# Kernel optimization log

Measured on AMD Instinct MI355X. Metric: run time of the kernel, lower is better.

The kernel has to match this reference:

```python
import jax, jax.numpy as jnp
import numpy as np

B = 4            # number of scenes (equal-size segments; offset = [M,2M,3M,4M])
K_NEAR = 16
K_FAR = 32
K_SMOOTH = 8
T_LOC = 0.1
T_CON = 0.5
BN_EPS = 1e-5


def setup_inputs() -> dict:
    key = jax.random.key(0)
    ks = jax.random.split(key, 8)
    N, C, H, O = 32768, 6, 64, 1
    coords = jax.random.uniform(ks[0], (N, 3), jnp.float32) * 2.0 - 1.0
    feat = jax.random.normal(ks[1], (N, C), jnp.float32)
    return {
        'feat': feat,
        'coords': coords,
        'W1': jax.random.normal(ks[2], (C, H), jnp.float32) * 0.1,
        'b1': jnp.zeros((H,), jnp.float32),
        'g1': jnp.ones((H,), jnp.float32),
        'be1': jnp.zeros((H,), jnp.float32),
        'W2': jax.random.normal(ks[3], (H, H), jnp.float32) * 0.1,
        'b2': jnp.zeros((H,), jnp.float32),
        'g2': jnp.ones((H,), jnp.float32),
        'be2': jnp.zeros((H,), jnp.float32),
        'W3': jax.random.normal(ks[4], (H, O), jnp.float32) * 0.1,
        'b3': jnp.zeros((O,), jnp.float32),
    }


def _bn_train(x, g, b):
    # BatchNorm1d in train mode: biased batch statistics
    mu = x.mean(axis=0)
    var = x.var(axis=0)
    return g * (x - mu) * jax.lax.rsqrt(var + BN_EPS) + b


def _knn_per_scene(c):
    # c: [M,3] -> [M,K_FAR] sorted nearest-neighbor indices (self first)
    sq = jnp.sum(c * c, axis=-1)                       # [M]
    d2 = sq[:, None] + sq[None, :] - 2.0 * (c @ c.T)   # [M,M] GEMM-based
    return jax.lax.top_k(-d2, K_FAR)[1]                # [M,K_FAR]


def _forward(feat, coords, W1, b1, g1, be1, W2, b2, g2, be2, W3, b3):
    N = feat.shape[0]
    M = N // B
    # ---- PointSorter MLP -> ordering scores in (0,1) ----
    h = jax.nn.gelu(_bn_train(feat @ W1 + b1, g1, be1), approximate=False)
    h = jax.nn.gelu(_bn_train(h @ W2 + b2, g2, be2), approximate=False)
    scores = jax.nn.sigmoid(h @ W3 + b3)               # [N, num_orders]
    s = scores.mean(axis=1, keepdims=True)             # [N,1] (scores_mean)
    # ---- single fused KNN (k=32); slice for k=16 (near) and k=8 (smooth) ----
    cb = coords.reshape(B, M, 3)
    idx = jax.vmap(_knn_per_scene)(cb)                 # [B,M,K_FAR] local
    idx = (idx + (jnp.arange(B) * M)[:, None, None]).reshape(N, K_FAR)
    idx_near = idx[:, :K_NEAR]
    idx_far = idx[:, K_NEAR:]
    idx_sm = idx[:, :K_SMOOTH]
    # ---- locality: neighbors should have similar scores ----
    sd = jnp.abs(s[:, None, :] - s[idx_near])[..., 0]          # [N,16]
    diff = coords[:, None, :] - coords[idx_near]               # [N,16,3]
    d = jnp.sqrt(jnp.maximum(jnp.sum(diff * diff, axis=2), 1e-24))
    w = jnp.exp(-d / T_LOC)
    loss_loc = jnp.sum(w * sd * sd) / jnp.maximum(jnp.sum(w), 1e-8)
    # ---- contrastive: far points should have different scores ----
    sim_pos = 1.0 - jnp.abs(s[:, None, :] - s[idx_near])       # [N,16,1]
    sim_neg = 1.0 - jnp.abs(s[:, None, :] - s[idx_far])        # [N,16,1]
    loss_pos = -jnp.mean(jnp.log(jax.nn.sigmoid(sim_pos / T_CON) + 1e-8))
    loss_neg = -jnp.mean(jnp.log(1.0 - jax.nn.sigmoid(sim_neg / T_CON) + 1e-8))
    loss_con = loss_pos + loss_neg
    # ---- smoothness: score close to mean of 8-NN scores ----
    nmean = s[idx_sm].mean(axis=1)                             # [N,1]
    loss_sm = jnp.mean((s - nmean) ** 2)
    return 1.0 * loss_loc + 0.5 * loss_con + 0.2 * loss_sm


def reference(feat, coords, W1, b1, g1, be1, W2, b2, g2, be2, W3, b3):
    return _forward(feat, coords, W1, b1, g1, be1, W2, b2, g2, be2, W3, b3)
```

## Files before the change

### kernel.cpp

```cpp
#include <hip/hip_runtime.h>

typedef unsigned long long u64;
typedef unsigned int u32;
typedef unsigned short u16;

#define N_PTS 32768
#define M_PTS 8192
#define C_IN 6
#define H_DIM 64

#define G 6
#define NCELL 216
#define NCELL_T 864
#define CW (1.0f/3.0f)

#define NBLK 256
#define NBLKD 1024
#define QG 4
#define NTASK (NCELL_T*2)
#define KTGT 48.0f

#define TL0 0.0494f
#define TL1 0.0740f
#define TL2 0.1110f
#define TL3 0.1736f
#define TL4 0.2600f
#define TL5 0.4000f

#define KEYMASK 0xFFFFE000u
#define IDXMASK 0x1FFFu


__device__ __forceinline__ float gelu_exact(float x) {
    return 0.5f * x * (1.0f + erff(x * 0.70710678118654752f));
}
__device__ __forceinline__ float sigmoidf_(float x) {
    return 1.0f / (1.0f + expf(-x));
}

__device__ __forceinline__ u32 bitonic_sort64_u32(u32 key, int lane) {
    #pragma unroll
    for (int k = 2; k <= 64; k <<= 1) {
        #pragma unroll
        for (int j = k >> 1; j; j >>= 1) {
            u32 pk = (u32)__shfl_xor((int)key, j, 64);
            bool up = ((lane & k) == 0);
            bool tmin = (((lane & j) == 0) == up);
            key = tmin ? min(key, pk) : max(key, pk);
        }
    }
    return key;
}

__device__ __forceinline__ void cell_geom(int cid, int lo[3], int hi[3],
        float lof[3], float hif[3], bool lw[3], bool hw[3]) {
    int cx = cid % G, cy = (cid / G) % G, cz = cid / (G*G);
    int ccrd[3] = {cx, cy, cz};
    bool wall[3]; int Wn = 0;
    #pragma unroll
    for (int d = 0; d < 3; ++d) { wall[d] = (ccrd[d] == 0 || ccrd[d] == G-1); Wn += wall[d]; }
    #pragma unroll
    for (int d = 0; d < 3; ++d) {
        if (Wn >= 2 && !wall[d]) { lo[d] = min(max(ccrd[d]-2, 0), G-5); hi[d] = lo[d]+4; }
        else                     { lo[d] = min(max(ccrd[d]-1, 0), G-3); hi[d] = lo[d]+2; }
    }
    #pragma unroll
    for (int d = 0; d < 3; ++d) {
        lof[d] = -1.0f + lo[d]*CW; hif[d] = -1.0f + (hi[d]+1)*CW;
        lw[d] = (lo[d] == 0); hw[d] = (hi[d] == G-1);
    }
}

__global__ __launch_bounds__(256) void kA(const float* __restrict__ feat,
        const float* __restrict__ coords, const float* __restrict__ W1,
        const float* __restrict__ b1, u32* __restrict__ gcount,
        u16* __restrict__ pcell, float* __restrict__ stats1) {
    __shared__ float red[512];
    int t = threadIdx.x, bid = blockIdx.x;
    if (bid < 128) {
        int n = bid * 256 + t;
        float x = coords[n*3], y = coords[n*3+1], z = coords[n*3+2];
        int cx = min(G-1, max(0, (int)floorf((x + 1.0f) * 3.0f)));
        int cy = min(G-1, max(0, (int)floorf((y + 1.0f) * 3.0f)));
        int cz = min(G-1, max(0, (int)floorf((z + 1.0f) * 3.0f)));
        int gcid = (n >> 13) * NCELL + (cz*G + cy)*G + cx;
        pcell[n] = (u16)gcid;
        atomicAdd(&gcount[gcid], 1u);
    }
    int c = t & 63, w = t >> 6;
    float w1c[C_IN];
    #pragma unroll
    for (int k = 0; k < C_IN; ++k) w1c[k] = W1[k*H_DIM + c];
    float bias = b1[c];
    float s1 = 0.f, s2 = 0.f;
    #pragma unroll 1
    for (int n = bid*8 + w*2; n < N_PTS; n += NBLK*8) {
        const float* fa = feat + n*C_IN;
        const float* fb = feat + (n+1)*C_IN;
        float ha = bias, hb = bias;
        #pragma unroll
        for (int k = 0; k < C_IN; ++k) {
            ha = fmaf(fa[k], w1c[k], ha);
            hb = fmaf(fb[k], w1c[k], hb);
        }
        s1 += ha + hb;
        s2 = fmaf(ha, ha, s2); s2 = fmaf(hb, hb, s2);
    }
    red[w*64 + c] = s1;
    red[256 + w*64 + c] = s2;
    __syncthreads();
    if (t < 64) {
        float a = red[t] + red[64+t] + red[128+t] + red[192+t];
        float b = red[256+t] + red[320+t] + red[384+t] + red[448+t];
        atomicAdd(&stats1[t], a);
        atomicAdd(&stats1[64+t], b);
    }
}

__global__ __launch_bounds__(256) void kB(const float* __restrict__ feat,
        const float* __restrict__ W1, const float* __restrict__ b1,
        const float* __restrict__ stats1, const float* __restrict__ g1,
        const float* __restrict__ be1, const float* __restrict__ W2,
        const float* __restrict__ b2, const u32* __restrict__ gcount,
        u32* __restrict__ cellstart, u32* __restrict__ cellptr,
        float* __restrict__ stats2) {
    __shared__ float red[512];
    __shared__ u32 sc[256];
    int t = threadIdx.x, bid = blockIdx.x;
    if (bid == 0) {
        u32 loc[4]; u32 s = 0;
        #pragma unroll
        for (int j = 0; j < 4; ++j) {
            int idx = t*4 + j;
            loc[j] = (idx < NCELL_T) ? gcount[idx] : 0u;
            s += loc[j];
        }
        sc[t] = s;
        __syncthreads();
        for (int off = 1; off < 256; off <<= 1) {
            u32 v = sc[t];
            if (t >= off) v += sc[t-off];
            __syncthreads();
            sc[t] = v;
            __syncthreads();
        }
        u32 run = sc[t] - s;
        #pragma unroll
        for (int j = 0; j < 4; ++j) {
            int idx = t*4 + j;
            if (idx < NCELL_T) { cellstart[idx] = run; cellptr[idx] = run; }
            run += loc[j];
        }
        if (t == 255) cellstart[NCELL_T] = sc[255];
        __syncthreads();
    }
    int c = t & 63, w = t >> 6;
    float w2c[H_DIM];
    #pragma unroll
    for (int k = 0; k < H_DIM; ++k) w2c[k] = W2[k*H_DIM + c];
    float w1c[C_IN];
    #pragma unroll
    for (int k = 0; k < C_IN; ++k) w1c[k] = W1[k*H_DIM + c];
    float mean1 = stats1[c] * (1.0f/N_PTS);
    float var1  = stats1[64+c] * (1.0f/N_PTS) - mean1*mean1;
    float sc1 = g1[c] * rsqrtf(var1 + 1e-5f);
    float sh1 = be1[c] - mean1*sc1;
    float bias1 = b1[c], bias2 = b2[c];
    float s1 = 0.f, s2 = 0.f;
    #pragma unroll 1
    for (int n = bid*16 + w*4; n < N_PTS; n += NBLK*16) {
        float h[4], a[4], h2[4];
        #pragma unroll
        for (int p = 0; p < 4; ++p) {
            const float* f = feat + (n+p)*C_IN;
            h[p] = bias1;
            #pragma unroll
            for (int k = 0; k < C_IN; ++k) h[p] = fmaf(f[k], w1c[k], h[p]);
            a[p] = gelu_exact(fmaf(sc1, h[p], sh1));
            h2[p] = bias2;
        }
        #pragma unroll
        for (int k = 0; k < H_DIM; ++k) {
            #pragma unroll
            for (int p = 0; p < 4; ++p)
                h2[p] = fmaf(__shfl(a[p], k, 64), w2c[k], h2[p]);
        }
        #pragma unroll
        for (int p = 0; p < 4; ++p) {
            s1 += h2[p];
            s2 = fmaf(h2[p], h2[p], s2);
        }
    }
    red[w*64 + c] = s1;
    red[256 + w*64 + c] = s2;
    __syncthreads();
    if (t < 64) {
        float a = red[t] + red[64+t] + red[128+t] + red[192+t];
        float b = red[256+t] + red[320+t] + red[384+t] + red[448+t];
        atomicAdd(&stats2[t], a);
        atomicAdd(&stats2[64+t], b);
    }
}

__global__ __launch_bounds__(256) void kC(const float* __restrict__ feat,
        const float* __restrict__ coords,
        const float* __restrict__ W1, const float* __restrict__ b1,
        const float* __restrict__ stats1, const float* __restrict__ g1,
        const float* __restrict__ be1, const float* __restrict__ W2,
        const float* __restrict__ b2, const float* __restrict__ stats2,
        const float* __restrict__ g2v, const float* __restrict__ be2,
        const float* __restrict__ W3, const float* __restrict__ b3,
        const u16* __restrict__ pcell, u32* __restrict__ cellptr,
        float4* __restrict__ P4s, float* __restrict__ S) {
    int t = threadIdx.x, bid = blockIdx.x;
    if (bid < 128) {
        int n = bid * 256 + t;
        float x = coords[n*3], y = coords[n*3+1], z = coords[n*3+2];
        u32 pos = atomicAdd(&cellptr[pcell[n]], 1u);
        P4s[pos] = make_float4(x, y, z, __uint_as_float((u32)(n & (M_PTS-1))));
    }
    int c = t & 63, w = t >> 6;
    float w2c[H_DIM];
    #pragma unroll
    for (int k = 0; k < H_DIM; ++k) w2c[k] = W2[k*H_DIM + c];
    float w1c[C_IN];
    #pragma unroll
    for (int k = 0; k < C_IN; ++k) w1c[k] = W1[k*H_DIM + c];
    float mean1 = stats1[c] * (1.0f/N_PTS);
    float var1  = stats1[64+c] * (1.0f/N_PTS) - mean1*mean1;
    float sc1 = g1[c] * rsqrtf(var1 + 1e-5f);
    float sh1 = be1[c] - mean1*sc1;
    float mean2 = stats2[c] * (1.0f/N_PTS);
    float var2  = stats2[64+c] * (1.0f/N_PTS) - mean2*mean2;
    float sc2 = g2v[c] * rsqrtf(var2 + 1e-5f);
    float sh2 = be2[c] - mean2*sc2;
    float bias1 = b1[c], bias2 = b2[c], w3 = W3[c], bb = b3[0];
    #pragma unroll 1
    for (int n = bid*16 + w*4; n < N_PTS; n += NBLK*16) {
        float h[4], a[4], h2[4];
        #pragma unroll
        for (int p = 0; p < 4; ++p) {
            const float* f = feat + (n+p)*C_IN;
            h[p] = bias1;
            #pragma unroll
            for (int k = 0; k < C_IN; ++k) h[p] = fmaf(f[k], w1c[k], h[p]);
            a[p] = gelu_exact(fmaf(sc1, h[p], sh1));
            h2[p] = bias2;
        }
        #pragma unroll
        for (int k = 0; k < H_DIM; ++k) {
            #pragma unroll
            for (int p = 0; p < 4; ++p)
                h2[p] = fmaf(__shfl(a[p], k, 64), w2c[k], h2[p]);
        }
        float v[4];
        #pragma unroll
        for (int p = 0; p < 4; ++p)
            v[p] = gelu_exact(fmaf(sc2, h2[p], sh2)) * w3;
        #pragma unroll
        for (int m = 32; m; m >>= 1) {
            #pragma unroll
            for (int p = 0; p < 4; ++p) v[p] += __shfl_xor(v[p], m, 64);
        }
        if (c == 0) {
            #pragma unroll
            for (int p = 0; p < 4; ++p) S[n+p] = sigmoidf_(v[p] + bb);
        }
    }
}

__global__ __launch_bounds__(256) void kD(const float4* __restrict__ P4s,
        const u32* __restrict__ cellstart, const float* __restrict__ S,
        double* __restrict__ accum, u32* __restrict__ donecnt,
        u32* __restrict__ taskctr, float* __restrict__ out) {
    __shared__ u32 wavebuf[4][QG][128];
    __shared__ int runsb[16], runse[16];
    __shared__ int nruns_s;
    __shared__ int curtask_s, nexttask_s;
    __shared__ u32 flistB[64];
    __shared__ u32 flnB;
    __shared__ int frunsb[16], frunse[16];
    __shared__ u32 cnt6[6];
    __shared__ u32 ovcnt;
    __shared__ float smacc;
    __shared__ double lred[4][5];

    int t = threadIdx.x;
    int lane = t & 63, w = t >> 6;
    u64 lmask = (1ull << lane) - 1ull;
    if (t == 0) { flnB = 0; curtask_s = (int)atomicAdd(taskctr, 1u); }
    __syncthreads();

    double anum=0.0, aden=0.0, aslp=0.0, asln=0.0, asmo=0.0;

    for (;;) {
        int tid = curtask_s;
        if (tid >= NTASK) break;
        if (t == 0) nexttask_s = (int)atomicAdd(taskctr, 1u);

        int cell = tid >> 1, part = tid & 1;
        int scene = cell / NCELL;
        int cid = cell - scene*NCELL;
        int sbase = scene * M_PTS;

        int lo[3], hi[3]; float lof[3], hif[3]; bool lw[3], hw[3];
        cell_geom(cid, lo, hi, lof, hif, lw, hw);
        if (t == 0) {
            int nr = 0;
            int nx = hi[0]-lo[0]+1;
            for (int z = lo[2]; z <= hi[2]; ++z)
                for (int y = lo[1]; y <= hi[1]; ++y) {
                    int bc = scene*NCELL + (z*G + y)*G + lo[0];
                    runsb[nr] = (int)cellstart[bc];
                    runse[nr] = (int)cellstart[bc + nx];
                    ++nr;
                }
            nruns_s = nr;
        }
        int gcid = scene*NCELL + cid;
        int qstart = (int)cellstart[gcid];
        int qn = (int)cellstart[gcid+1] - qstart;
        __syncthreads();
        int nruns = nruns_s;
        int hq = (qn + 1) >> 1;
        int hqs = qstart + part * hq;
        int hqn = qn - part * hq; if (hqn > hq) hqn = hq; if (hqn < 0) hqn = 0;

        for (int g0 = w*QG; g0 < hqn; g0 += 4*QG) {
            int jcount = min(QG, hqn - g0);
            int qb = hqs + g0;
            float qx[QG], qy[QG], qz[QG], qs[QG], tp[QG];
            u32 qid[QG], baseq[QG];
            #pragma unroll
            for (int j = 0; j < QG; ++j) {
                int qg = qb + min(j, jcount-1);
                float4 qc = P4s[qg];
                qx[j]=qc.x; qy[j]=qc.y; qz[j]=qc.z;
                qid[j] = __float_as_uint(qc.w);
                float qsq = fmaf(qc.x, qc.x, fmaf(qc.y, qc.y, qc.z*qc.z));
                qs[j] = qsq;
                float cov = 1e9f;
                float qdv[3] = {qc.x, qc.y, qc.z};
                #pragma unroll
                for (int d = 0; d < 3; ++d) {
                    if (!lw[d]) cov = fminf(cov, qdv[d] - lof[d]);
                    if (!hw[d]) cov = fminf(cov, hif[d] - qdv[d]);
                }
                float g2 = cov*cov;
                float axx = fminf(qc.x+1.f, 1.f-qc.x);
                float ayy = fminf(qc.y+1.f, 1.f-qc.y);
                float azz = fminf(qc.z+1.f, 1.f-qc.z);
                float r = 0.224f;
                #pragma unroll
                for (int it = 0; it < 3; ++it) {
                    float ir = 1.0f / r;
                    float ux = fminf(axx*ir, 1.f), uy = fminf(ayy*ir, 1.f), uz = fminf(azz*ir, 1.f);
                    float fx = 0.25f*(2.f + 3.f*ux - ux*ux*ux);
                    float fy = 0.25f*(2.f + 3.f*uy - uy*uy*uy);
                    float fz = 0.25f*(2.f + 3.f*uz - uz*uz*uz);
                    r = cbrtf(KTGT / (4289.32f * fx * fy * fz));
                }
                tp[j] = (j < jcount) ? (fminf(r*r, g2) - qsq) : -1e30f;
                baseq[j] = 0;
            }

            for (int rr = 0; rr < nruns; ++rr) {
                int ve = runse[rr];
                for (int v0 = runsb[rr]; v0 < ve; v0 += 128) {
                    int vA = v0 + lane, vB = v0 + 64 + lane;
                    bool okA = vA < ve, okB = vB < ve;
                    float4 pA = make_float4(1e3f,1e3f,1e3f,0.f);
                    float4 pB = make_float4(1e3f,1e3f,1e3f,0.f);
                    if (okA) pA = P4s[vA];
                    if (okB) pB = P4s[vB];
                    float sqA = fmaf(pA.x, pA.x, fmaf(pA.y, pA.y, pA.z*pA.z));
                    float sqB = fmaf(pB.x, pB.x, fmaf(pB.y, pB.y, pB.z*pB.z));
                    #pragma unroll
                    for (int j = 0; j < QG; ++j) {
                        float dotA = fmaf(qx[j], pA.x, fmaf(qy[j], pA.y, qz[j]*pA.z));
                        float e2A = fmaf(-2.0f, dotA, sqA);
                        bool prA = okA && (e2A < tp[j]);
                        u64 mkA = __ballot(prA);
                        if (prA) {
                            float d2 = fmaxf(e2A + qs[j], 0.0f);
                            u32 key = (__float_as_uint(d2) & KEYMASK) | __float_as_uint(pA.w);
                            u32 pos = baseq[j] + (u32)__popcll(mkA & lmask);
                            if (pos < 128u) wavebuf[w][j][pos] = key;
                        }
                        baseq[j] += (u32)__popcll(mkA);
                        float dotB = fmaf(qx[j], pB.x, fmaf(qy[j], pB.y, qz[j]*pB.z));
                        float e2B = fmaf(-2.0f, dotB, sqB);
                        bool prB = okB && (e2B < tp[j]);
                        u64 mkB = __ballot(prB);
                        if (prB) {
                            float d2 = fmaxf(e2B + qs[j], 0.0f);
                            u32 key = (__float_as_uint(d2) & KEYMASK) | __float_as_uint(pB.w);
                            u32 pos = baseq[j] + (u32)__popcll(mkB & lmask);
                            if (pos < 128u) wavebuf[w][j][pos] = key;
                        }
                        baseq[j] += (u32)__popcll(mkB);
                    }
                }
            }

            #pragma unroll 1
            for (int j = 0; j < QG; ++j) {
                if (j >= jcount) continue;
                int qg = qb + j;
                u32 M = baseq[j];
                if (M < 32u || M > 128u) {
                    if (lane == 0) {
                        u32 idx = atomicAdd(&flnB, 1u);
                        if (idx < 64u) flistB[idx] = ((u32)cell << 16) | (u32)qg;
                    }
                    continue;
                }
                u32 k0 = (lane < (int)min(M, 64u)) ? wavebuf[w][j][lane] : 0xFFFFFFFFu;
                k0 = bitonic_sort64_u32(k0, lane);
                if (M > 64u) {
                    u32 k1 = (lane < (int)(M - 64u)) ? wavebuf[w][j][64 + lane] : 0xFFFFFFFFu;
                    k1 = bitonic_sort64_u32(k1, lane);
                    u32 pk = (u32)__shfl((int)k1, 63 - lane, 64);
                    u32 lo2 = min(k0, pk);
                    #pragma unroll
                    for (int jj = 32; jj; jj >>= 1) {
                        u32 pj = (u32)__shfl_xor((int)lo2, jj, 64);
                        lo2 = ((lane & jj) == 0) ? min(lo2, pj) : max(lo2, pj);
                    }
                    k0 = lo2;
                }
                float si = S[sbase + (int)qid[j]];
                float smsum = 0.f;
                if (lane < 32) {
                    float d2 = __uint_as_float(k0 & KEYMASK);
                    u32 jo = k0 & IDXMASK;
                    float sj = S[sbase + (int)jo];
                    float sd = fabsf(si - sj);
                    float sim = 1.0f - sd;
                    if (lane < 16) {
                        float d = sqrtf(fmaxf(d2, 1e-24f));
                        float wgt = expf(-10.0f*d);
                        anum += (double)(wgt*sd*sd);
                        aden += (double)wgt;
                        aslp += (double)logf(sigmoidf_(2.0f*sim) + 1e-8f);
                        if (lane < 8) smsum += sj;
                    } else {
                        asln += (double)logf(sigmoidf_(-2.0f*sim) + 1e-8f);
                    }
                }
                #pragma unroll
                for (int m = 32; m; m >>= 1) smsum += __shfl_xor(smsum, m, 64);
                if (lane == 0) {
                    float dd = si - smsum*0.125f;
                    asmo += (double)(dd*dd);
                }
            }
        }
        __syncthreads();
        if (t == 0) curtask_s = nexttask_s;
        __syncthreads();
    }
    __syncthreads();

    int nf = min((int)flnB, 64);
    u32* ovbuf = &wavebuf[0][0][0];
    for (int f = 0; f < nf; ++f) {
        u32 ent = flistB[f];
        int fqg = (int)(ent & 0xFFFFu);
        int fcell = (int)(ent >> 16);
        int scene = fcell / NCELL;
        int cid = fcell - scene*NCELL;
        int sbase = scene * M_PTS;
        int lo[3], hi[3]; float lof[3], hif[3]; bool lw[3], hw[3];
        cell_geom(cid, lo, hi, lof, hif, lw, hw);
        int nx = hi[0]-lo[0]+1, ny = hi[1]-lo[1]+1, nz = hi[2]-lo[2]+1;
        int nruns = ny*nz;
        if (t < nruns) {
            int yy = t % ny, zz = t / ny;
            int bc = scene*NCELL + ((lo[2]+zz)*G + (lo[1]+yy))*G + lo[0];
            frunsb[t] = (int)cellstart[bc];
            frunse[t] = (int)cellstart[bc + nx];
        }
        float4 fqc = P4s[fqg];
        float fsq = fmaf(fqc.x, fqc.x, fmaf(fqc.y, fqc.y, fqc.z*fqc.z));
        float fcov = 1e9f;
        float fqd[3] = {fqc.x, fqc.y, fqc.z};
        #pragma unroll
        for (int d = 0; d < 3; ++d) {
            if (!lw[d]) fcov = fminf(fcov, fqd[d] - lof[d]);
            if (!hw[d]) fcov = fminf(fcov, hif[d] - fqd[d]);
        }
        float fg2 = fcov*fcov;
        if (t < 6) cnt6[t] = 0;
        if (t == 0) { ovcnt = 0; smacc = 0.f; }
        __syncthreads();
        u32 c0=0,c1=0,c2=0,c3=0,c4=0,c5=0;
        for (int rr = 0; rr < nruns; ++rr) {
            for (int v = frunsb[rr] + t; v < frunse[rr]; v += 256) {
                float4 pp = P4s[v];
                float sq = fmaf(pp.x, pp.x, fmaf(pp.y, pp.y, pp.z*pp.z));
                float dot = fmaf(fqc.x, pp.x, fmaf(fqc.y, pp.y, fqc.z*pp.z));
                float e2 = fmaf(-2.0f, dot, sq);
                c0 += (e2 < TL0-fsq); c1 += (e2 < TL1-fsq); c2 += (e2 < TL2-fsq);
                c3 += (e2 < TL3-fsq); c4 += (e2 < TL4-fsq); c5 += (e2 < TL5-fsq);
            }
        }
        #pragma unroll
        for (int m = 32; m; m >>= 1) {
            c0 += __shfl_xor(c0, m, 64); c1 += __shfl_xor(c1, m, 64);
            c2 += __shfl_xor(c2, m, 64); c3 += __shfl_xor(c3, m, 64);
            c4 += __shfl_xor(c4, m, 64); c5 += __shfl_xor(c5, m, 64);
        }
        if ((t & 63) == 0) {
            atomicAdd(&cnt6[0], c0); atomicAdd(&cnt6[1], c1);
            atomicAdd(&cnt6[2], c2); atomicAdd(&cnt6[3], c3);
            atomicAdd(&cnt6[4], c4); atomicAdd(&cnt6[5], c5);
        }
        __syncthreads();
        float tau = TL2;
        if (TL3 <= fg2) tau = TL3;
        if (TL4 <= fg2) tau = TL4;
        if (TL5 <= fg2) tau = TL5;
        if      (cnt6[0] >= 32u) tau = TL0;
        else if (cnt6[1] >= 32u) tau = TL1;
        else if (cnt6[2] >= 32u) tau = TL2;
        else if (TL3 <= fg2 && cnt6[3] >= 32u) tau = TL3;
        else if (TL4 <= fg2 && cnt6[4] >= 32u) tau = TL4;
        else if (TL5 <= fg2 && cnt6[5] >= 32u) tau = TL5;
        float ftp = tau - fsq;
        for (int rr = 0; rr < nruns; ++rr) {
            for (int v = frunsb[rr] + t; v < frunse[rr]; v += 256) {
                float4 pp = P4s[v];
                float sq = fmaf(pp.x, pp.x, fmaf(pp.y, pp.y, pp.z*pp.z));
                float dot = fmaf(fqc.x, pp.x, fmaf(fqc.y, pp.y, fqc.z*pp.z));
                float e2 = fmaf(-2.0f, dot, sq);
                if (e2 < ftp) {
                    float d2 = fmaxf(e2 + fsq, 0.0f);
                    u32 key = (__float_as_uint(d2) & KEYMASK) | __float_as_uint(pp.w);
                    u32 pos = atomicAdd(&ovcnt, 1u);
                    if (pos < 2048u) ovbuf[pos] = key;
                }
            }
        }
        __syncthreads();
        u32 Mf = min(ovcnt, 2048u);
        float fsi = S[sbase + (int)__float_as_uint(fqc.w)];
        for (int i = t; i < (int)Mf; i += 256) {
            u32 mykey = ovbuf[i];
            u32 rank = 0;
            for (u32 jj = 0; jj < Mf; ++jj) rank += (ovbuf[jj] < mykey);
            if (rank < 32u) {
                float d2 = __uint_as_float(mykey & KEYMASK);
                u32 jo = mykey & IDXMASK;
                float sj = S[sbase + (int)jo];
                float sd = fabsf(fsi - sj);
                float sim = 1.0f - sd;
                if (rank < 16u) {
                    float d = sqrtf(fmaxf(d2, 1e-24f));
                    float wgt = expf(-10.0f*d);
                    anum += (double)(wgt*sd*sd);
                    aden += (double)wgt;
                    aslp += (double)logf(sigmoidf_(2.0f*sim) + 1e-8f);
                    if (rank < 8u) atomicAdd(&smacc, sj);
                } else {
                    asln += (double)logf(sigmoidf_(-2.0f*sim) + 1e-8f);
                }
            }
        }
        __syncthreads();
        if (t == 0) {
            float dd = fsi - smacc*0.125f;
            asmo += (double)(dd*dd);
        }
        __syncthreads();
    }

    double v[5] = {anum, aden, aslp, asln, asmo};
    #pragma unroll
    for (int k = 0; k < 5; ++k) {
        for (int m = 32; m; m >>= 1) v[k] += __shfl_xor(v[k], m, 64);
    }
    if (lane == 0) {
        #pragma unroll
        for (int k = 0; k < 5; ++k) lred[w][k] = v[k];
    }
    __syncthreads();
    if (t == 0) {
        #pragma unroll
        for (int k = 0; k < 5; ++k)
            atomicAdd(&accum[k], lred[0][k] + lred[1][k] + lred[2][k] + lred[3][k]);
        __threadfence();
        u32 old = atomicAdd(donecnt, 1u);
        if (old == (u32)(NBLKD - 1)) {
            double a0 = atomicAdd(&accum[0], 0.0);
            double a1 = atomicAdd(&accum[1], 0.0);
            double a2 = atomicAdd(&accum[2], 0.0);
            double a3 = atomicAdd(&accum[3], 0.0);
            double a4 = atomicAdd(&accum[4], 0.0);
            double loss_loc = a0 / fmax(a1, 1e-8);
            double inv = 1.0 / ((double)N_PTS * 16.0);
            double loss_con = -(a2 * inv) - (a3 * inv);
            double loss_sm = a4 / (double)N_PTS;
            out[0] = (float)(loss_loc + 0.5*loss_con + 0.2*loss_sm);
        }
    }
}

extern "C" void kernel_launch(void* const* d_in, const int* in_sizes, int n_in,
                              void* d_out, int out_size, void* d_ws, size_t ws_size,
                              hipStream_t stream) {
    const float* feat   = (const float*)d_in[0];
    const float* coords = (const float*)d_in[1];
    const float* W1 = (const float*)d_in[2];
    const float* b1 = (const float*)d_in[3];
    const float* g1 = (const float*)d_in[4];
    const float* be1= (const float*)d_in[5];
    const float* W2 = (const float*)d_in[6];
    const float* b2 = (const float*)d_in[7];
    const float* g2 = (const float*)d_in[8];
    const float* be2= (const float*)d_in[9];
    const float* W3 = (const float*)d_in[10];
    const float* b3 = (const float*)d_in[11];
    char* ws = (char*)d_ws;

    float* stats1   = (float*)(ws);
    float* stats2   = (float*)(ws + 512);
    u32* gcount     = (u32*)(ws + 1024);
    double* accum   = (double*)(ws + 4480);
    u32* donecnt    = (u32*)(ws + 4520);
    u32* taskctr    = (u32*)(ws + 4524);
    u32* cellstart  = (u32*)(ws + 4544);
    u32* cellptr    = (u32*)(ws + 8008);
    float* S        = (float*)(ws + 11472);
    float4* P4s     = (float4*)(ws + 142544);
    u16* pcell      = (u16*)(ws + 666832);

    hipMemsetAsync(d_ws, 0, 4544, stream);

    hipLaunchKernelGGL(kA, dim3(NBLK), dim3(256), 0, stream,
                       feat, coords, W1, b1, gcount, pcell, stats1);
    hipLaunchKernelGGL(kB, dim3(NBLK), dim3(256), 0, stream,
                       feat, W1, b1, stats1, g1, be1, W2, b2,
                       gcount, cellstart, cellptr, stats2);
    hipLaunchKernelGGL(kC, dim3(NBLK), dim3(256), 0, stream,
                       feat, coords, W1, b1, stats1, g1, be1, W2, b2,
                       stats2, g2, be2, W3, b3, pcell, cellptr, P4s, S);
    hipLaunchKernelGGL(kD, dim3(NBLKD), dim3(256), 0, stream,
                       P4s, cellstart, S, accum, donecnt, taskctr, (float*)d_out);
}
```

Baseline: 315.6 us.

## Split KNN cell tasks into four query groups and vectorize feature loads

Each KNN cell task is now split into four query chunks of 16 points instead of two halves, with the last chunk taking any remaining points. Chunks with no queries exit early, and the dynamic block count rises to match. The aim is finer-grained load balancing across the work-stealing task queue. Separately, feature rows are read as three float2 loads in the MLP kernels, which assumes 8-byte alignment (row stride is 6 floats, so this holds). The trade-off is that each task still loads its neighbour-run list, so that setup and the sync overhead are repeated per task, and last-chunk sizes can be uneven.

```diff
diff --git a/kernel.cpp b/kernel.cpp
--- a/kernel.cpp
+++ b/kernel.cpp
@@ -15,9 +15,10 @@
 #define CW (1.0f/3.0f)
 
 #define NBLK 256
-#define NBLKD 1024
+#define NBLKD 1792
 #define QG 4
-#define NTASK (NCELL_T*2)
+#define GPC 4
+#define NTASK (NCELL_T*GPC)
 #define KTGT 48.0f
 
 #define TL0 0.0494f
@@ -95,14 +96,17 @@
     float s1 = 0.f, s2 = 0.f;
     #pragma unroll 1
     for (int n = bid*8 + w*2; n < N_PTS; n += NBLK*8) {
-        const float* fa = feat + n*C_IN;
-        const float* fb = feat + (n+1)*C_IN;
+        const float2* fa = (const float2*)(feat + n*C_IN);
+        const float2* fb = (const float2*)(feat + (n+1)*C_IN);
+        float2 a0 = fa[0], a1 = fa[1], a2 = fa[2];
+        float2 b0 = fb[0], b1v = fb[1], b2v = fb[2];
         float ha = bias, hb = bias;
-        #pragma unroll
-        for (int k = 0; k < C_IN; ++k) {
-            ha = fmaf(fa[k], w1c[k], ha);
-            hb = fmaf(fb[k], w1c[k], hb);
-        }
+        ha = fmaf(a0.x, w1c[0], ha); ha = fmaf(a0.y, w1c[1], ha);
+        ha = fmaf(a1.x, w1c[2], ha); ha = fmaf(a1.y, w1c[3], ha);
+        ha = fmaf(a2.x, w1c[4], ha); ha = fmaf(a2.y, w1c[5], ha);
+        hb = fmaf(b0.x, w1c[0], hb); hb = fmaf(b0.y, w1c[1], hb);
+        hb = fmaf(b1v.x, w1c[2], hb); hb = fmaf(b1v.y, w1c[3], hb);
+        hb = fmaf(b2v.x, w1c[4], hb); hb = fmaf(b2v.y, w1c[5], hb);
         s1 += ha + hb;
         s2 = fmaf(ha, ha, s2); s2 = fmaf(hb, hb, s2);
     }
@@ -172,10 +176,12 @@
         float h[4], a[4], h2[4];
         #pragma unroll
         for (int p = 0; p < 4; ++p) {
-            const float* f = feat + (n+p)*C_IN;
+            const float2* f2 = (const float2*)(feat + (n+p)*C_IN);
+            float2 x0 = f2[0], x1 = f2[1], x2 = f2[2];
             h[p] = bias1;
-            #pragma unroll
-            for (int k = 0; k < C_IN; ++k) h[p] = fmaf(f[k], w1c[k], h[p]);
+            h[p] = fmaf(x0.x, w1c[0], h[p]); h[p] = fmaf(x0.y, w1c[1], h[p]);
+            h[p] = fmaf(x1.x, w1c[2], h[p]); h[p] = fmaf(x1.y, w1c[3], h[p]);
+            h[p] = fmaf(x2.x, w1c[4], h[p]); h[p] = fmaf(x2.y, w1c[5], h[p]);
             a[p] = gelu_exact(fmaf(sc1, h[p], sh1));
             h2[p] = bias2;
         }
@@ -240,10 +246,12 @@
         float h[4], a[4], h2[4];
         #pragma unroll
         for (int p = 0; p < 4; ++p) {
-            const float* f = feat + (n+p)*C_IN;
+            const float2* f2 = (const float2*)(feat + (n+p)*C_IN);
+            float2 x0 = f2[0], x1 = f2[1], x2 = f2[2];
             h[p] = bias1;
-            #pragma unroll
-            for (int k = 0; k < C_IN; ++k) h[p] = fmaf(f[k], w1c[k], h[p]);
+            h[p] = fmaf(x0.x, w1c[0], h[p]); h[p] = fmaf(x0.y, w1c[1], h[p]);
+            h[p] = fmaf(x1.x, w1c[2], h[p]); h[p] = fmaf(x1.y, w1c[3], h[p]);
+            h[p] = fmaf(x2.x, w1c[4], h[p]); h[p] = fmaf(x2.y, w1c[5], h[p]);
             a[p] = gelu_exact(fmaf(sc1, h[p], sh1));
             h2[p] = bias2;
         }
@@ -298,10 +306,22 @@
         if (tid >= NTASK) break;
         if (t == 0) nexttask_s = (int)atomicAdd(taskctr, 1u);
 
-        int cell = tid >> 1, part = tid & 1;
+        int cell = tid >> 2, g = tid & 3;
         int scene = cell / NCELL;
         int cid = cell - scene*NCELL;
         int sbase = scene * M_PTS;
+
+        int gcid = scene*NCELL + cid;
+        int qstart = (int)cellstart[gcid];
+        int qn = (int)cellstart[gcid+1] - qstart;
+        int qlo = g * 16;
+        if (qlo >= qn) {
+            __syncthreads();
+            if (t == 0) curtask_s = nexttask_s;
+            __syncthreads();
+            continue;
+        }
+        int qhiEnd = (g == GPC-1) ? qn : min(qlo + 16, qn);
 
         int lo[3], hi[3]; float lof[3], hif[3]; bool lw[3], hw[3];
         cell_geom(cid, lo, hi, lof, hif, lw, hw);
@@ -317,18 +337,12 @@
                 }
             nruns_s = nr;
         }
-        int gcid = scene*NCELL + cid;
-        int qstart = (int)cellstart[gcid];
-        int qn = (int)cellstart[gcid+1] - qstart;
         __syncthreads();
         int nruns = nruns_s;
-        int hq = (qn + 1) >> 1;
-        int hqs = qstart + part * hq;
-        int hqn = qn - part * hq; if (hqn > hq) hqn = hq; if (hqn < 0) hqn = 0;
-
-        for (int g0 = w*QG; g0 < hqn; g0 += 4*QG) {
-            int jcount = min(QG, hqn - g0);
-            int qb = hqs + g0;
+
+        for (int g0 = qstart + qlo + w*QG; g0 < qstart + qhiEnd; g0 += 16) {
+            int jcount = min(QG, qstart + qhiEnd - g0);
+            int qb = g0;
             float qx[QG], qy[QG], qz[QG], qs[QG], tp[QG];
             u32 qid[QG], baseq[QG];
             #pragma unroll
```

Result: slower. 390.8 us (+23.8%).
